# Kernel optimization log

Hardware: AMD Instinct MI355X
Metric: run time of the kernel (lower is better)

## Reference

```python
import jax, jax.numpy as jnp
import numpy as np

N_NODES = 50000
N_EDGES = 800000
D = 128        # input_dim == output_dim
D_EDGE = 64    # edge_attr_size
Z_DIM = 2 * D + D_EDGE  # 320


def setup_inputs() -> dict:
    key = jax.random.key(0)
    k1, k2, k3, k4, k5 = jax.random.split(key, 5)
    x = jax.random.normal(k1, (N_NODES, D), dtype=jnp.float32)
    edge_index = jax.random.randint(k2, (2, N_EDGES), 0, N_NODES, dtype=jnp.int64)
    edge_attr = jax.random.normal(k3, (N_EDGES, D_EDGE), dtype=jnp.float32)
    scale = 1.0 / np.sqrt(Z_DIM)
    W_f = jax.random.normal(k4, (Z_DIM, D), dtype=jnp.float32) * scale
    W_s = jax.random.normal(k5, (Z_DIM, D), dtype=jnp.float32) * scale
    b_f = jnp.zeros((D,), dtype=jnp.float32)
    b_s = jnp.zeros((D,), dtype=jnp.float32)
    return {"x": x, "edge_index": edge_index, "edge_attr": edge_attr,
            "W_f": W_f, "b_f": b_f, "W_s": W_s, "b_s": b_s}


def reference(x, edge_index, edge_attr, W_f, b_f, W_s, b_s):
    # Dropout(p=0.0) is identity in inference.
    src = edge_index[0]  # j (message source)
    dst = edge_index[1]  # i (message target)
    # z_e = [x_i, x_j, e_ij]  -> [E, 2D + D_edge]
    z = jnp.concatenate([x[dst], x[src], edge_attr], axis=-1)
    # CGConv message: sigmoid(lin_f(z)) * softplus(lin_s(z))
    msg = jax.nn.sigmoid(z @ W_f + b_f) * jax.nn.softplus(z @ W_s + b_s)
    # scatter-add aggregation + residual
    out = jax.ops.segment_sum(msg, dst, num_segments=x.shape[0]) + x
    # use_activation=True -> ReLU
    return jax.nn.relu(out)
```

## Files before the change

### kernel.cpp

```cpp
#include <hip/hip_runtime.h>
#include <hip/hip_bf16.h>

#define E_TOTAL   800000
#define NN        50000
#define DD        128
#define DE        64
#define ZDIM      320
#define KE        192
#define MT        64
#define NBS       196

typedef short bf16x8 __attribute__((ext_vector_type(8)));
typedef float f32x4  __attribute__((ext_vector_type(4)));

__device__ __forceinline__ unsigned short f2bf(float f) {
    union { float f; unsigned int u; } v; v.f = f;
    unsigned int u = v.u;
    return (unsigned short)((u + 0x7fffu + ((u >> 16) & 1u)) >> 16);
}

__device__ __forceinline__ float bf2f(unsigned short h) {
    union { unsigned u; float f; } v; v.u = ((unsigned)h) << 16; return v.f;
}

__device__ __forceinline__ unsigned pkbf2(float a, float b) {
    __hip_bfloat162 h = __float22bfloat162_rn(make_float2(a, b));
    unsigned u; __builtin_memcpy(&u, &h, 4); return u;
}

__device__ __forceinline__ uint2 pkbf4(float4 v) {
    uint2 r; r.x = pkbf2(v.x, v.y); r.y = pkbf2(v.z, v.w); return r;
}

__device__ __forceinline__ float fast_rcp(float x) {
#if __has_builtin(__builtin_amdgcn_rcpf)
    return __builtin_amdgcn_rcpf(x);
#else
    return 1.0f / x;
#endif
}


__global__ void prep_kernel(const float* __restrict__ x,
                            const int* __restrict__ ei,
                            const float* __restrict__ W_f,
                            const float* __restrict__ W_s,
                            unsigned short* __restrict__ WtE,
                            unsigned short* __restrict__ WtN,
                            int* __restrict__ counts,
                            float* __restrict__ out) {
    int id = blockIdx.x * 256 + threadIdx.x;
    ((float4*)out)[id] = ((const float4*)x)[id];
    if (id < E_TOTAL) atomicAdd(&counts[ei[E_TOTAL + id]], 1);
    if (id < 256 * KE) {
        int n = id / KE, k = id - n * KE;
        int ok = 128 + k;
        float wv = (n < DD) ? W_f[ok * DD + n] : W_s[ok * DD + (n - DD)];
        WtE[id] = f2bf(wv);
    } else if (id < 256 * KE + 256 * DD) {
        int id2 = id - 256 * KE;
        int n = id2 / DD, k = id2 - n * DD;
        float wv = (n < DD) ? W_f[k * DD + n] : W_s[k * DD + (n - DD)];
        WtN[id2] = f2bf(wv);
    }
}

__global__ void scan_part(const int* __restrict__ counts, int* __restrict__ partial) {
    __shared__ int red[256];
    int t = threadIdx.x, k = blockIdx.x * 256 + t;
    red[t] = (k < NN) ? counts[k] : 0;
    __syncthreads();
    for (int d = 128; d > 0; d >>= 1) {
        if (t < d) red[t] += red[t + d];
        __syncthreads();
    }
    if (t == 0) partial[blockIdx.x] = red[0];
}

__global__ void scan_top(int* __restrict__ partial) {
    __shared__ int s[256];
    int t = threadIdx.x;
    int v = (t < NBS) ? partial[t] : 0;
    s[t] = v; __syncthreads();
    for (int d = 1; d < 256; d <<= 1) {
        int a = (t >= d) ? s[t - d] : 0;
        __syncthreads();
        s[t] += a;
        __syncthreads();
    }
    if (t < NBS) partial[t] = s[t] - v;
}

__global__ void scan_final(const int* __restrict__ counts,
                           const int* __restrict__ partial,
                           int* __restrict__ cursor) {
    __shared__ int s[256];
    int t = threadIdx.x, k = blockIdx.x * 256 + t;
    int v = (k < NN) ? counts[k] : 0;
    s[t] = v; __syncthreads();
    for (int d = 1; d < 256; d <<= 1) {
        int a = (t >= d) ? s[t - d] : 0;
        __syncthreads();
        s[t] += a;
        __syncthreads();
    }
    if (k < NN) cursor[k] = partial[blockIdx.x] + s[t] - v;
}

__global__ void scatter_kernel(const int* __restrict__ ei, int* __restrict__ cursor,
                               uint2* __restrict__ spak2) {
    int e = blockIdx.x * 256 + threadIdx.x;
    if (e < E_TOTAL) {
        int d = ei[E_TOTAL + e];
        int pos = atomicAdd(&cursor[d], 1);
        uint2 p; p.x = ((unsigned)d << 16) | (unsigned)ei[e]; p.y = (unsigned)e;
        spak2[pos] = p;
    }
}

__global__ __launch_bounds__(256, 4)
void node_kernel(const float* __restrict__ x,
                 const unsigned short* __restrict__ WtN,
                 const float* __restrict__ bf_, const float* __restrict__ bs_,
                 unsigned short* __restrict__ nodeP) {
    __shared__ unsigned short A_lds[MT * DD];
    const int t = threadIdx.x;
    const int m_off = blockIdx.x * MT;
    const int lane = t & 63, w = t >> 6, l15 = lane & 15, quad = lane >> 4;

    #pragma unroll
    for (int it = 0; it < 8; ++it) {
        int idx = it * 256 + t;
        int e = idx >> 5, kq = idx & 31;
        int row = m_off + e; if (row >= NN) row = NN - 1;
        float4 v = ((const float4*)(x + (size_t)row * DD))[kq];
        int g = kq >> 1;
        int col = ((g & ~7) | ((g & 7) ^ (e & 7))) * 8 + (kq & 1) * 4;
        *((uint2*)&A_lds[e * DD + col]) = pkbf4(v);
    }

    f32x4 acc[4][4] = {};
    const int nt0 = 2 * w;
    const unsigned short* Bp[4];
    #pragma unroll
    for (int u = 0; u < 4; ++u) {
        int nt = nt0 + ((u < 2) ? u : (6 + u));
        Bp[u] = WtN + (size_t)(nt * 16 + l15) * DD + quad * 8;
    }
    __syncthreads();

    #pragma unroll
    for (int ks = 0; ks < 4; ++ks) {
        bf16x8 af[4], bfr[4];
        #pragma unroll
        for (int i = 0; i < 4; ++i) {
            int m = i * 16 + l15;
            int g = 4 * ks + quad;
            int col = ((g & ~7) | ((g & 7) ^ (l15 & 7))) * 8;
            af[i] = *((const bf16x8*)&A_lds[m * DD + col]);
        }
        #pragma unroll
        for (int u = 0; u < 4; ++u)
            bfr[u] = *((const bf16x8*)(Bp[u] + ks * 32));
        #pragma unroll
        for (int i = 0; i < 4; ++i)
            #pragma unroll
            for (int u = 0; u < 4; ++u)
                acc[i][u] = __builtin_amdgcn_mfma_f32_16x16x32_bf16(
                    af[i], bfr[u], acc[i][u], 0, 0, 0);
    }

    const int c0 = 32 * w + l15, c1 = c0 + 16;
    const float bf0 = bf_[c0], bs0 = bs_[c0], bf1 = bf_[c1], bs1 = bs_[c1];
    #pragma unroll
    for (int i = 0; i < 4; ++i)
        #pragma unroll
        for (int j = 0; j < 4; ++j) {
            int e = i * 16 + quad * 4 + j;
            int row = m_off + e;
            if (row < NN) {
                uint2 pk;
                pk.x = pkbf2(acc[i][0][j] + bf0, acc[i][1][j] + bf1);
                pk.y = pkbf2(acc[i][2][j] + bs0, acc[i][3][j] + bs1);
                *((uint2*)(nodeP + (size_t)row * 256 + w * 64 + l15 * 4)) = pk;
            }
        }
}

__global__ __launch_bounds__(256, 4)
void edge_kernel(const float* __restrict__ x,
                 const float* __restrict__ ea,
                 const unsigned short* __restrict__ WtE,
                 const unsigned short* __restrict__ nodeP,
                 float* __restrict__ out,
                 const uint2* __restrict__ spak2) {
    __shared__ unsigned short A_lds[MT * KE];
    __shared__ int dst_lds[MT];
    __shared__ int src_lds[MT];
    __shared__ int eid_lds[MT];

    const int t = threadIdx.x;
    const int m_off = blockIdx.x * MT;
    const int lane = t & 63, w = t >> 6, l15 = lane & 15, quad = lane >> 4;

    if (t < MT) {
        uint2 p = spak2[m_off + t];
        dst_lds[t] = (int)(p.x >> 16);
        src_lds[t] = (int)(p.x & 0xffffu);
        eid_lds[t] = (int)p.y;
    }
    __syncthreads();

    #pragma unroll
    for (int it = 0; it < 4; ++it) {
        int idx = it * 256 + t;
        int e = idx >> 4, kq = idx & 15;
        float4 v = ((const float4*)(ea + (size_t)eid_lds[e] * DE))[kq];
        int g = 16 + (kq >> 1);
        int col = ((g & ~7) | ((g & 7) ^ (e & 7))) * 8 + (kq & 1) * 4;
        *((uint2*)&A_lds[e * KE + col]) = pkbf4(v);
    }
    #pragma unroll
    for (int it = 0; it < 8; ++it) {
        int idx = it * 256 + t;
        int e = idx >> 5, kq = idx & 31;
        float4 v = ((const float4*)(x + (size_t)src_lds[e] * DD))[kq];
        int g = kq >> 1;
        int col = ((g & ~7) | ((g & 7) ^ (e & 7))) * 8 + (kq & 1) * 4;
        *((uint2*)&A_lds[e * KE + col]) = pkbf4(v);
    }

    f32x4 acc[4][4] = {};
    const int nt0 = 2 * w;
    const unsigned short* Bp[4];
    #pragma unroll
    for (int u = 0; u < 4; ++u) {
        int nt = nt0 + ((u < 2) ? u : (6 + u));
        Bp[u] = WtE + (size_t)(nt * 16 + l15) * KE + quad * 8;
    }
    __syncthreads();

    #pragma unroll
    for (int ks = 0; ks < 6; ++ks) {
        bf16x8 af[4], bfr[4];
        #pragma unroll
        for (int i = 0; i < 4; ++i) {
            int m = i * 16 + l15;
            int g = 4 * ks + quad;
            int col = ((g & ~7) | ((g & 7) ^ (l15 & 7))) * 8;
            af[i] = *((const bf16x8*)&A_lds[m * KE + col]);
        }
        #pragma unroll
        for (int u = 0; u < 4; ++u)
            bfr[u] = *((const bf16x8*)(Bp[u] + ks * 32));
        #pragma unroll
        for (int i = 0; i < 4; ++i)
            #pragma unroll
            for (int u = 0; u < 4; ++u)
                acc[i][u] = __builtin_amdgcn_mfma_f32_16x16x32_bf16(
                    af[i], bfr[u], acc[i][u], 0, 0, 0);
    }

    const int c0 = 32 * w + l15, c1 = c0 + 16;
    const int np_off = w * 64 + l15 * 4;

    int d = -1;
    float s0 = 0.f, s1 = 0.f, nf0 = 0.f, ns0 = 0.f, nf1 = 0.f, ns1 = 0.f;
    #pragma unroll
    for (int i = 0; i < 4; ++i)
        #pragma unroll
        for (int j = 0; j < 4; ++j) {
            int e = i * 16 + quad * 4 + j;
            int dd = dst_lds[e];
            if (dd != d) {
                if (d >= 0) {
                    atomicAdd(out + (size_t)d * DD + c0, s0);
                    atomicAdd(out + (size_t)d * DD + c1, s1);
                }
                d = dd; s0 = 0.f; s1 = 0.f;
                uint2 pk = *((const uint2*)(nodeP + (size_t)d * 256 + np_off));
                nf0 = bf2f((unsigned short)(pk.x & 0xffffu));
                nf1 = bf2f((unsigned short)(pk.x >> 16));
                ns0 = bf2f((unsigned short)(pk.y & 0xffffu));
                ns1 = bf2f((unsigned short)(pk.y >> 16));
            }
            float f0  = acc[i][0][j] + nf0;
            float sg0 = acc[i][2][j] + ns0;
            s0 += fast_rcp(1.f + __expf(-f0)) *
                  (fmaxf(sg0, 0.f) + __logf(1.f + __expf(-fabsf(sg0))));
            float f1  = acc[i][1][j] + nf1;
            float sg1 = acc[i][3][j] + ns1;
            s1 += fast_rcp(1.f + __expf(-f1)) *
                  (fmaxf(sg1, 0.f) + __logf(1.f + __expf(-fabsf(sg1))));
        }
    atomicAdd(out + (size_t)d * DD + c0, s0);
    atomicAdd(out + (size_t)d * DD + c1, s1);
}

__global__ void relu_kernel(float* __restrict__ out) {
    int id = blockIdx.x * 256 + threadIdx.x;
    if (id < NN * DD / 4) {
        float4 v = ((float4*)out)[id];
        v.x = fmaxf(v.x, 0.0f); v.y = fmaxf(v.y, 0.0f);
        v.z = fmaxf(v.z, 0.0f); v.w = fmaxf(v.w, 0.0f);
        ((float4*)out)[id] = v;
    }
}


__global__ void prep_fb(const float* __restrict__ x,
                        const float* __restrict__ W_f,
                        const float* __restrict__ W_s,
                        unsigned short* __restrict__ Wt,
                        float* __restrict__ out) {
    int id = blockIdx.x * 256 + threadIdx.x;
    if (id < NN * DD / 4)
        ((float4*)out)[id] = ((const float4*)x)[id];
    if (id < 2 * DD * ZDIM) {
        int n = id / ZDIM, k = id - n * ZDIM;
        float wv = (n < DD) ? W_f[k * DD + n] : W_s[k * DD + (n - DD)];
        Wt[n * ZDIM + k] = f2bf(wv);
    }
}

__global__ __launch_bounds__(256, 3)
void edge_fb(const float* __restrict__ x,
             const int* __restrict__ ei,
             const float* __restrict__ ea,
             const unsigned short* __restrict__ Wt,
             const float* __restrict__ bf_,
             const float* __restrict__ bs_,
             float* __restrict__ out) {
    __shared__ unsigned short A_lds[MT * ZDIM];
    __shared__ int dst_lds[MT];
    __shared__ int src_lds[MT];

    const int t = threadIdx.x;
    const int m_off = blockIdx.x * MT;
    const int lane = t & 63, w = t >> 6, l15 = lane & 15, quad = lane >> 4;

    if (t < MT) dst_lds[t] = ei[E_TOTAL + m_off + t];
    else if (t < 2 * MT) src_lds[t - MT] = ei[m_off + (t - MT)];
    __syncthreads();

    #pragma unroll
    for (int it = 0; it < 4; ++it) {
        int idx = it * 256 + t;
        int e = idx >> 4, kq = idx & 15;
        float4 v = ((const float4*)(ea + (size_t)(m_off + e) * DE))[kq];
        int g = 32 + (kq >> 1);
        int col = ((g & ~7) | ((g & 7) ^ (e & 7))) * 8 + (kq & 1) * 4;
        *((uint2*)&A_lds[e * ZDIM + col]) = pkbf4(v);
    }
    #pragma unroll
    for (int it = 0; it < 8; ++it) {
        int idx = it * 256 + t;
        int e = idx >> 5, kq = idx & 31;
        float4 v = ((const float4*)(x + (size_t)dst_lds[e] * DD))[kq];
        int g = kq >> 1;
        int col = ((g & ~7) | ((g & 7) ^ (e & 7))) * 8 + (kq & 1) * 4;
        *((uint2*)&A_lds[e * ZDIM + col]) = pkbf4(v);
    }
    #pragma unroll
    for (int it = 0; it < 8; ++it) {
        int idx = it * 256 + t;
        int e = idx >> 5, kq = idx & 31;
        float4 v = ((const float4*)(x + (size_t)src_lds[e] * DD))[kq];
        int g = 16 + (kq >> 1);
        int col = ((g & ~7) | ((g & 7) ^ (e & 7))) * 8 + (kq & 1) * 4;
        *((uint2*)&A_lds[e * ZDIM + col]) = pkbf4(v);
    }

    f32x4 acc[4][4] = {};
    const int nt0 = 2 * w;
    const unsigned short* Bp[4];
    #pragma unroll
    for (int u = 0; u < 4; ++u) {
        int nt = nt0 + ((u < 2) ? u : (6 + u));
        Bp[u] = Wt + (size_t)(nt * 16 + l15) * ZDIM + quad * 8;
    }
    __syncthreads();

    #pragma unroll
    for (int ks = 0; ks < 10; ++ks) {
        bf16x8 af[4], bfr[4];
        #pragma unroll
        for (int i = 0; i < 4; ++i) {
            int m = i * 16 + l15;
            int g = 4 * ks + quad;
            int col = ((g & ~7) | ((g & 7) ^ (l15 & 7))) * 8;
            af[i] = *((const bf16x8*)&A_lds[m * ZDIM + col]);
        }
        #pragma unroll
        for (int u = 0; u < 4; ++u)
            bfr[u] = *((const bf16x8*)(Bp[u] + ks * 32));
        #pragma unroll
        for (int i = 0; i < 4; ++i)
            #pragma unroll
            for (int u = 0; u < 4; ++u)
                acc[i][u] = __builtin_amdgcn_mfma_f32_16x16x32_bf16(
                    af[i], bfr[u], acc[i][u], 0, 0, 0);
    }

    const int c0 = 32 * w + l15, c1 = c0 + 16;
    const float bf0 = bf_[c0], bs0 = bs_[c0], bf1 = bf_[c1], bs1 = bs_[c1];
    #pragma unroll
    for (int i = 0; i < 4; ++i)
        #pragma unroll
        for (int j = 0; j < 4; ++j) {
            int e = i * 16 + quad * 4 + j;
            float* op = out + (size_t)dst_lds[e] * DD;
            float f0 = acc[i][0][j] + bf0;
            float sg0 = acc[i][2][j] + bs0;
            atomicAdd(op + c0, fast_rcp(1.f + __expf(-f0)) *
                (fmaxf(sg0, 0.f) + __logf(1.f + __expf(-fabsf(sg0)))));
            float f1 = acc[i][1][j] + bf1;
            float sg1 = acc[i][3][j] + bs1;
            atomicAdd(op + c1, fast_rcp(1.f + __expf(-f1)) *
                (fmaxf(sg1, 0.f) + __logf(1.f + __expf(-fabsf(sg1)))));
        }
}


extern "C" void kernel_launch(void* const* d_in, const int* in_sizes, int n_in,
                              void* d_out, int out_size, void* d_ws, size_t ws_size,
                              hipStream_t stream) {
    (void)in_sizes; (void)n_in; (void)out_size;
    const float* x   = (const float*)d_in[0];
    const int*   ei  = (const int*)d_in[1];
    const float* ea  = (const float*)d_in[2];
    const float* W_f = (const float*)d_in[3];
    const float* b_f = (const float*)d_in[4];
    const float* W_s = (const float*)d_in[5];
    const float* b_s = (const float*)d_in[6];
    float* out = (float*)d_out;

    char* ws = (char*)d_ws;
    unsigned short* WtE    = (unsigned short*)ws;
    unsigned short* WtN    = (unsigned short*)(ws + 98304);
    int*            counts = (int*)(ws + 163840);
    int*            cursor = (int*)(ws + 363840);
    int*            partial= (int*)(ws + 563840);
    uint2*          spak2  = (uint2*)(ws + 564864);
    unsigned short* nodeP  = (unsigned short*)(ws + 6964864);
    const size_t WS_NEED = 32564864;

    if (ws_size >= WS_NEED) {
        hipMemsetAsync(counts, 0, NN * sizeof(int), stream);
        prep_kernel<<<NN * DD / 4 / 256, 256, 0, stream>>>(
            x, ei, W_f, W_s, WtE, WtN, counts, out);
        scan_part<<<NBS, 256, 0, stream>>>(counts, partial);
        scan_top<<<1, 256, 0, stream>>>(partial);
        scan_final<<<NBS, 256, 0, stream>>>(counts, partial, cursor);
        scatter_kernel<<<(E_TOTAL + 255) / 256, 256, 0, stream>>>(ei, cursor, spak2);
        node_kernel<<<(NN + MT - 1) / MT, 256, 0, stream>>>(x, WtN, b_f, b_s, nodeP);
        edge_kernel<<<E_TOTAL / MT, 256, 0, stream>>>(
            x, ea, WtE, nodeP, out, spak2);
    } else {
        unsigned short* Wt = (unsigned short*)ws;
        prep_fb<<<6250, 256, 0, stream>>>(x, W_f, W_s, Wt, out);
        edge_fb<<<E_TOTAL / MT, 256, 0, stream>>>(x, ei, ea, Wt, b_f, b_s, out);
    }

    relu_kernel<<<6250, 256, 0, stream>>>(out);
}
```

Baseline: 668.6 us.

## Precompute per-node projections for both source and destination features in edge path

Result: faster. 621.5 us (-7.0%).

```diff
diff --git a/kernel.cpp b/kernel.cpp
--- a/kernel.cpp
+++ b/kernel.cpp
@@ -38,6 +38,275 @@
 #else
     return 1.0f / x;
 #endif
+}
+
+
+__global__ void scan_part(const int* __restrict__ counts, int* __restrict__ partial) {
+    __shared__ int red[256];
+    int t = threadIdx.x, k = blockIdx.x * 256 + t;
+    red[t] = (k < NN) ? counts[k] : 0;
+    __syncthreads();
+    for (int d = 128; d > 0; d >>= 1) {
+        if (t < d) red[t] += red[t + d];
+        __syncthreads();
+    }
+    if (t == 0) partial[blockIdx.x] = red[0];
+}
+
+__global__ void scan_top(int* __restrict__ partial) {
+    __shared__ int s[256];
+    int t = threadIdx.x;
+    int v = (t < NBS) ? partial[t] : 0;
+    s[t] = v; __syncthreads();
+    for (int d = 1; d < 256; d <<= 1) {
+        int a = (t >= d) ? s[t - d] : 0;
+        __syncthreads();
+        s[t] += a;
+        __syncthreads();
+    }
+    if (t < NBS) partial[t] = s[t] - v;
+}
+
+__global__ void scan_final(const int* __restrict__ counts,
+                           const int* __restrict__ partial,
+                           int* __restrict__ cursor) {
+    __shared__ int s[256];
+    int t = threadIdx.x, k = blockIdx.x * 256 + t;
+    int v = (k < NN) ? counts[k] : 0;
+    s[t] = v; __syncthreads();
+    for (int d = 1; d < 256; d <<= 1) {
+        int a = (t >= d) ? s[t - d] : 0;
+        __syncthreads();
+        s[t] += a;
+        __syncthreads();
+    }
+    if (k < NN) cursor[k] = partial[blockIdx.x] + s[t] - v;
+}
+
+__global__ void scatter_kernel(const int* __restrict__ ei, int* __restrict__ cursor,
+                               uint2* __restrict__ spak2) {
+    int e = blockIdx.x * 256 + threadIdx.x;
+    if (e < E_TOTAL) {
+        int d = ei[E_TOTAL + e];
+        int pos = atomicAdd(&cursor[d], 1);
+        uint2 p; p.x = ((unsigned)d << 16) | (unsigned)ei[e]; p.y = (unsigned)e;
+        spak2[pos] = p;
+    }
+}
+
+
+__global__ void prep_kernel2(const float* __restrict__ x,
+                             const int* __restrict__ ei,
+                             const float* __restrict__ W_f,
+                             const float* __restrict__ W_s,
+                             unsigned short* __restrict__ WtE,
+                             unsigned short* __restrict__ WtN,
+                             int* __restrict__ counts,
+                             float* __restrict__ out) {
+    int id = blockIdx.x * 256 + threadIdx.x;
+    ((float4*)out)[id] = ((const float4*)x)[id];
+    if (id < E_TOTAL) atomicAdd(&counts[ei[E_TOTAL + id]], 1);
+    if (id < 256 * DE) {
+        int n = id >> 6, k = id & 63;
+        int ok = 2 * DD + k;
+        float wv = (n < DD) ? W_f[ok * DD + n] : W_s[ok * DD + (n - DD)];
+        WtE[id] = f2bf(wv);
+    } else if (id < 256 * DE + 2 * 256 * DD) {
+        int id2 = id - 256 * DE;
+        int part = id2 >> 15;
+        int r = id2 & 32767;
+        int n = r >> 7, k = r & 127;
+        int ok = part * DD + k;
+        float wv = (n < DD) ? W_f[ok * DD + n] : W_s[ok * DD + (n - DD)];
+        WtN[id2] = f2bf(wv);
+    }
+}
+
+__global__ __launch_bounds__(256, 4)
+void node_kernel2(const float* __restrict__ x,
+                  const unsigned short* __restrict__ WtN,
+                  const float* __restrict__ bf_, const float* __restrict__ bs_,
+                  unsigned short* __restrict__ nodeP) {
+    __shared__ unsigned short A_lds[MT * DD];
+    const int t = threadIdx.x;
+    const int m_off = blockIdx.x * MT;
+    const int part = blockIdx.y;
+    const int lane = t & 63, w = t >> 6, l15 = lane & 15, quad = lane >> 4;
+
+    #pragma unroll
+    for (int it = 0; it < 8; ++it) {
+        int idx = it * 256 + t;
+        int e = idx >> 5, kq = idx & 31;
+        int row = m_off + e; if (row >= NN) row = NN - 1;
+        float4 v = ((const float4*)(x + (size_t)row * DD))[kq];
+        int g = kq >> 1;
+        int col = ((g & ~7) | ((g & 7) ^ (e & 7))) * 8 + (kq & 1) * 4;
+        *((uint2*)&A_lds[e * DD + col]) = pkbf4(v);
+    }
+
+    f32x4 acc[4][4] = {};
+    const int nt0 = 2 * w;
+    const unsigned short* Bp[4];
+    #pragma unroll
+    for (int u = 0; u < 4; ++u) {
+        int nt = nt0 + ((u < 2) ? u : (6 + u));
+        Bp[u] = WtN + (size_t)part * (256 * DD) + (size_t)(nt * 16 + l15) * DD + quad * 8;
+    }
+    __syncthreads();
+
+    #pragma unroll
+    for (int ks = 0; ks < 4; ++ks) {
+        bf16x8 af[4], bfr[4];
+        #pragma unroll
+        for (int i = 0; i < 4; ++i) {
+            int m = i * 16 + l15;
+            int g = 4 * ks + quad;
+            int col = ((g & ~7) | ((g & 7) ^ (l15 & 7))) * 8;
+            af[i] = *((const bf16x8*)&A_lds[m * DD + col]);
+        }
+        #pragma unroll
+        for (int u = 0; u < 4; ++u)
+            bfr[u] = *((const bf16x8*)(Bp[u] + ks * 32));
+        #pragma unroll
+        for (int i = 0; i < 4; ++i)
+            #pragma unroll
+            for (int u = 0; u < 4; ++u)
+                acc[i][u] = __builtin_amdgcn_mfma_f32_16x16x32_bf16(
+                    af[i], bfr[u], acc[i][u], 0, 0, 0);
+    }
+
+    const int c0 = 32 * w + l15, c1 = c0 + 16;
+    const float bf0 = part ? 0.f : bf_[c0], bs0 = part ? 0.f : bs_[c0];
+    const float bf1 = part ? 0.f : bf_[c1], bs1 = part ? 0.f : bs_[c1];
+    #pragma unroll
+    for (int i = 0; i < 4; ++i)
+        #pragma unroll
+        for (int j = 0; j < 4; ++j) {
+            int e = i * 16 + quad * 4 + j;
+            int row = m_off + e;
+            if (row < NN) {
+                uint2 pk;
+                pk.x = pkbf2(acc[i][0][j] + bf0, acc[i][1][j] + bf1);
+                pk.y = pkbf2(acc[i][2][j] + bs0, acc[i][3][j] + bs1);
+                *((uint2*)(nodeP + (size_t)row * 512 + part * 256 + w * 64 + l15 * 4)) = pk;
+            }
+        }
+}
+
+#define PS_LOAD(PS, I)                                                          \
+    _Pragma("unroll")                                                           \
+    for (int j = 0; j < 4; ++j)                                                 \
+        PS[j] = *((const uint2*)(npS + (size_t)src_lds[(I) * 16 + quad * 4 + j] * 512));
+
+#define PS_PROC(PS, I)                                                          \
+    _Pragma("unroll")                                                           \
+    for (int j = 0; j < 4; ++j) {                                               \
+        int e = (I) * 16 + quad * 4 + j;                                        \
+        int dd = dst_lds[e];                                                    \
+        if (dd != d) {                                                          \
+            if (d >= 0) {                                                       \
+                atomicAdd(out + (size_t)d * DD + c0, s0);                       \
+                atomicAdd(out + (size_t)d * DD + c1, s1);                       \
+            }                                                                   \
+            d = dd; s0 = 0.f; s1 = 0.f;                                         \
+            uint2 pk = *((const uint2*)(nodeP + (size_t)d * 512 + np_off));     \
+            nf0 = bf2f((unsigned short)(pk.x & 0xffffu));                       \
+            nf1 = bf2f((unsigned short)(pk.x >> 16));                           \
+            ns0 = bf2f((unsigned short)(pk.y & 0xffffu));                       \
+            ns1 = bf2f((unsigned short)(pk.y >> 16));                           \
+        }                                                                       \
+        uint2 pp = PS[j];                                                       \
+        float f0  = acc[(I)][0][j] + nf0 + bf2f((unsigned short)(pp.x & 0xffffu)); \
+        float f1  = acc[(I)][1][j] + nf1 + bf2f((unsigned short)(pp.x >> 16));  \
+        float sg0 = acc[(I)][2][j] + ns0 + bf2f((unsigned short)(pp.y & 0xffffu)); \
+        float sg1 = acc[(I)][3][j] + ns1 + bf2f((unsigned short)(pp.y >> 16));  \
+        s0 += fast_rcp(1.f + __expf(-f0)) *                                     \
+              (fmaxf(sg0, 0.f) + __logf(1.f + __expf(-fabsf(sg0))));            \
+        s1 += fast_rcp(1.f + __expf(-f1)) *                                     \
+              (fmaxf(sg1, 0.f) + __logf(1.f + __expf(-fabsf(sg1))));            \
+    }
+
+__global__ __launch_bounds__(256, 4)
+void edge_kernel2(const float* __restrict__ ea,
+                  const unsigned short* __restrict__ WtE,
+                  const unsigned short* __restrict__ nodeP,
+                  float* __restrict__ out,
+                  const uint2* __restrict__ spak2) {
+    __shared__ unsigned short A_lds[MT * DE];
+    __shared__ int dst_lds[MT];
+    __shared__ int src_lds[MT];
+    __shared__ int eid_lds[MT];
+
+    const int t = threadIdx.x;
+    const int m_off = blockIdx.x * MT;
+    const int lane = t & 63, w = t >> 6, l15 = lane & 15, quad = lane >> 4;
+
+    if (t < MT) {
+        uint2 p = spak2[m_off + t];
+        dst_lds[t] = (int)(p.x >> 16);
+        src_lds[t] = (int)(p.x & 0xffffu);
+        eid_lds[t] = (int)p.y;
+    }
+    __syncthreads();
+
+    #pragma unroll
+    for (int it = 0; it < 4; ++it) {
+        int idx = it * 256 + t;
+        int e = idx >> 4, kq = idx & 15;
+        float4 v = ((const float4*)(ea + (size_t)eid_lds[e] * DE))[kq];
+        int g = kq >> 1;
+        int col = ((g & 7) ^ (e & 7)) * 8 + (kq & 1) * 4;
+        *((uint2*)&A_lds[e * DE + col]) = pkbf4(v);
+    }
+
+    f32x4 acc[4][4] = {};
+    const int nt0 = 2 * w;
+    const unsigned short* Bp[4];
+    #pragma unroll
+    for (int u = 0; u < 4; ++u) {
+        int nt = nt0 + ((u < 2) ? u : (6 + u));
+        Bp[u] = WtE + (size_t)(nt * 16 + l15) * DE + quad * 8;
+    }
+    __syncthreads();
+
+    #pragma unroll
+    for (int ks = 0; ks < 2; ++ks) {
+        bf16x8 af[4], bfr[4];
+        #pragma unroll
+        for (int i = 0; i < 4; ++i) {
+            int m = i * 16 + l15;
+            int g = 4 * ks + quad;
+            int col = ((g & 7) ^ (l15 & 7)) * 8;
+            af[i] = *((const bf16x8*)&A_lds[m * DE + col]);
+        }
+        #pragma unroll
+        for (int u = 0; u < 4; ++u)
+            bfr[u] = *((const bf16x8*)(Bp[u] + ks * 32));
+        #pragma unroll
+        for (int i = 0; i < 4; ++i)
+            #pragma unroll
+            for (int u = 0; u < 4; ++u)
+                acc[i][u] = __builtin_amdgcn_mfma_f32_16x16x32_bf16(
+                    af[i], bfr[u], acc[i][u], 0, 0, 0);
+    }
+
+    const int c0 = 32 * w + l15, c1 = c0 + 16;
+    const int np_off = w * 64 + l15 * 4;
+    const unsigned short* npS = nodeP + 256 + np_off;
+
+    int d = -1;
+    float s0 = 0.f, s1 = 0.f, nf0 = 0.f, ns0 = 0.f, nf1 = 0.f, ns1 = 0.f;
+    uint2 psA[4], psB[4];
+    PS_LOAD(psA, 0)
+    PS_LOAD(psB, 1)
+    PS_PROC(psA, 0)
+    PS_LOAD(psA, 2)
+    PS_PROC(psB, 1)
+    PS_LOAD(psB, 3)
+    PS_PROC(psA, 2)
+    PS_PROC(psB, 3)
+    atomicAdd(out + (size_t)d * DD + c0, s0);
+    atomicAdd(out + (size_t)d * DD + c1, s1);
 }
 
 
@@ -62,59 +331,6 @@
         int n = id2 / DD, k = id2 - n * DD;
         float wv = (n < DD) ? W_f[k * DD + n] : W_s[k * DD + (n - DD)];
         WtN[id2] = f2bf(wv);
-    }
-}
-
-__global__ void scan_part(const int* __restrict__ counts, int* __restrict__ partial) {
-    __shared__ int red[256];
-    int t = threadIdx.x, k = blockIdx.x * 256 + t;
-    red[t] = (k < NN) ? counts[k] : 0;
-    __syncthreads();
-    for (int d = 128; d > 0; d >>= 1) {
-        if (t < d) red[t] += red[t + d];
-        __syncthreads();
-    }
-    if (t == 0) partial[blockIdx.x] = red[0];
-}
-
-__global__ void scan_top(int* __restrict__ partial) {
-    __shared__ int s[256];
-    int t = threadIdx.x;
-    int v = (t < NBS) ? partial[t] : 0;
-    s[t] = v; __syncthreads();
-    for (int d = 1; d < 256; d <<= 1) {
-        int a = (t >= d) ? s[t - d] : 0;
-        __syncthreads();
-        s[t] += a;
-        __syncthreads();
-    }
-    if (t < NBS) partial[t] = s[t] - v;
-}
-
-__global__ void scan_final(const int* __restrict__ counts,
-                           const int* __restrict__ partial,
-                           int* __restrict__ cursor) {
-    __shared__ int s[256];
-    int t = threadIdx.x, k = blockIdx.x * 256 + t;
-    int v = (k < NN) ? counts[k] : 0;
-    s[t] = v; __syncthreads();
-    for (int d = 1; d < 256; d <<= 1) {
-        int a = (t >= d) ? s[t - d] : 0;
-        __syncthreads();
-        s[t] += a;
-        __syncthreads();
-    }
-    if (k < NN) cursor[k] = partial[blockIdx.x] + s[t] - v;
-}
-
-__global__ void scatter_kernel(const int* __restrict__ ei, int* __restrict__ cursor,
-                               uint2* __restrict__ spak2) {
-    int e = blockIdx.x * 256 + threadIdx.x;
-    if (e < E_TOTAL) {
-        int d = ei[E_TOTAL + e];
-        int pos = atomicAdd(&cursor[d], 1);
-        uint2 p; p.x = ((unsigned)d << 16) | (unsigned)ei[e]; p.y = (unsigned)e;
-        spak2[pos] = p;
     }
 }
 
@@ -436,16 +652,38 @@
     float* out = (float*)d_out;
 
     char* ws = (char*)d_ws;
-    unsigned short* WtE    = (unsigned short*)ws;
-    unsigned short* WtN    = (unsigned short*)(ws + 98304);
-    int*            counts = (int*)(ws + 163840);
-    int*            cursor = (int*)(ws + 363840);
-    int*            partial= (int*)(ws + 563840);
-    uint2*          spak2  = (uint2*)(ws + 564864);
-    unsigned short* nodeP  = (unsigned short*)(ws + 6964864);
-    const size_t WS_NEED = 32564864;
-
-    if (ws_size >= WS_NEED) {
+    const size_t WS_NEED2 = 58164864;
+    const size_t WS_NEED1 = 32564864;
+
+    if (ws_size >= WS_NEED2) {
+        unsigned short* WtE2   = (unsigned short*)ws;
+        unsigned short* WtN2   = (unsigned short*)(ws + 32768);
+        int*            counts = (int*)(ws + 163840);
+        int*            cursor = (int*)(ws + 363840);
+        int*            partial= (int*)(ws + 563840);
+        uint2*          spak2  = (uint2*)(ws + 564864);
+        unsigned short* nodeP  = (unsigned short*)(ws + 6964864);
+
+        hipMemsetAsync(counts, 0, NN * sizeof(int), stream);
+        prep_kernel2<<<NN * DD / 4 / 256, 256, 0, stream>>>(
+            x, ei, W_f, W_s, WtE2, WtN2, counts, out);
+        scan_part<<<NBS, 256, 0, stream>>>(counts, partial);
+        scan_top<<<1, 256, 0, stream>>>(partial);
+        scan_final<<<NBS, 256, 0, stream>>>(counts, partial, cursor);
+        scatter_kernel<<<(E_TOTAL + 255) / 256, 256, 0, stream>>>(ei, cursor, spak2);
+        dim3 ng((NN + MT - 1) / MT, 2);
+        node_kernel2<<<ng, 256, 0, stream>>>(x, WtN2, b_f, b_s, nodeP);
+        edge_kernel2<<<E_TOTAL / MT, 256, 0, stream>>>(
+            ea, WtE2, nodeP, out, spak2);
+    } else if (ws_size >= WS_NEED1) {
+        unsigned short* WtE    = (unsigned short*)ws;
+        unsigned short* WtN    = (unsigned short*)(ws + 98304);
+        int*            counts = (int*)(ws + 163840);
+        int*            cursor = (int*)(ws + 363840);
+        int*            partial= (int*)(ws + 563840);
+        uint2*          spak2  = (uint2*)(ws + 564864);
+        unsigned short* nodeP  = (unsigned short*)(ws + 6964864);
+
         hipMemsetAsync(counts, 0, NN * sizeof(int), stream);
         prep_kernel<<<NN * DD / 4 / 256, 256, 0, stream>>>(
             x, ei, W_f, W_s, WtE, WtN, counts, out);
```
